# Kernel optimization log

Hardware: AMD Instinct MI355X
Metric: run time of the kernel (lower is better)

Reference implementation:

```python
import jax, jax.numpy as jnp
import numpy as np

N_NODES = 50000
N_EDGES = 800000
IN_DIM = 128
OUT_DIM = 64


def setup_inputs() -> dict:
    key = jax.random.key(0)
    k1, k2, k3, k4, k5, k6 = jax.random.split(key, 6)
    x = jax.random.normal(k1, (N_NODES, IN_DIM), dtype=jnp.float32)
    edge_row = jax.random.randint(k2, (N_EDGES,), 0, N_NODES, dtype=jnp.int32)
    edge_col = jax.random.randint(k3, (N_EDGES,), 0, N_NODES, dtype=jnp.int32)
    edge_val = jax.random.uniform(k4, (N_EDGES,), dtype=jnp.float32)
    stdv = 1.0 / np.sqrt(OUT_DIM)
    w = jax.random.uniform(k5, (IN_DIM, OUT_DIM), minval=-stdv, maxval=stdv, dtype=jnp.float32)
    b = jax.random.uniform(k6, (OUT_DIM,), minval=-stdv, maxval=stdv, dtype=jnp.float32)
    return {"x": x, "edge_row": edge_row, "edge_col": edge_col, "edge_val": edge_val, "w": w, "b": b}


def reference(x, edge_row, edge_col, edge_val, w, b):
    # dense projection: [N, in_dim] @ [in_dim, out_dim] -> [N, out_dim]
    hidden = x @ w
    # SpMM: out[r] = sum_e val[e] * hidden[col[e]] for edges with row[e] == r
    msg = hidden[edge_col] * edge_val[:, None]          # [E, out_dim]
    out = jax.ops.segment_sum(msg, edge_row, num_segments=N_NODES)
    return jax.nn.relu(out + b)
```

## Files before the change

kernel.cpp:

```cpp
#include <hip/hip_runtime.h>

#define N_NODES 50000
#define N_EDGES 800000
#define IN_DIM 128
#define OUT_DIM 64
#define CAP 64
#define PARTS 8
#define ROWS_PER_PART 6250
#define EDGES_PER_CHUNK 3125

#define GEMM_BLOCKS 784
#define BUCKET_BLOCKS (256 * PARTS)
#define TOTAL_BLOCKS (GEMM_BLOCKS + BUCKET_BLOCKS)

#define OFF_HID 0u
#define OFF_DEG 6400000u
#define OFF_BKT 6600192u

typedef short short8 __attribute__((ext_vector_type(8)));
typedef float f32x4 __attribute__((ext_vector_type(4)));
typedef float f32x2 __attribute__((ext_vector_type(2)));

__device__ __forceinline__ unsigned short bf_rne(float f) {
    unsigned u = __float_as_uint(f);
    u += 0x7fffu + ((u >> 16) & 1u);
    return (unsigned short)(u >> 16);
}
__device__ __forceinline__ float bf_lo(unsigned u) { return __uint_as_float(u << 16); }
__device__ __forceinline__ float bf_hi(unsigned u) { return __uint_as_float(u & 0xffff0000u); }

__global__ __launch_bounds__(256) void fused_kernel(
        const float* __restrict__ x, const float* __restrict__ w,
        unsigned short* __restrict__ hidb,
        const int* __restrict__ erow, const int* __restrict__ ecol,
        const float* __restrict__ eval,
        int* __restrict__ deg, int2* __restrict__ bucket) {
    if (blockIdx.x >= GEMM_BLOCKS) {
        const int bb = blockIdx.x - GEMM_BLOCKS;
        const int part = bb & (PARTS - 1);
        const int chunk = bb >> 3;
        const int rlo = part * ROWS_PER_PART;
        const int e0 = chunk * EDGES_PER_CHUNK;
        int i = threadIdx.x;
        #pragma unroll 1
        for (int trip = 0; trip < 3; ++trip, i += 1024) {
            const int eA = e0 + i,        eB = e0 + i + 256;
            const int eC = e0 + i + 512,  eD = e0 + i + 768;
            const int rA = __builtin_nontemporal_load(&erow[eA]);
            const int rB = __builtin_nontemporal_load(&erow[eB]);
            const int rC = __builtin_nontemporal_load(&erow[eC]);
            const int rD = __builtin_nontemporal_load(&erow[eD]);
            const int cA = __builtin_nontemporal_load(&ecol[eA]);
            const int cB = __builtin_nontemporal_load(&ecol[eB]);
            const int cC = __builtin_nontemporal_load(&ecol[eC]);
            const int cD = __builtin_nontemporal_load(&ecol[eD]);
            const float vA = __builtin_nontemporal_load(&eval[eA]);
            const float vB = __builtin_nontemporal_load(&eval[eB]);
            const float vC = __builtin_nontemporal_load(&eval[eC]);
            const float vD = __builtin_nontemporal_load(&eval[eD]);
            if ((unsigned)(rA - rlo) < (unsigned)ROWS_PER_PART) {
                const int pos = atomicAdd(&deg[rA], 1);
                if (pos < CAP) bucket[(size_t)rA * CAP + pos] = make_int2(cA, __float_as_int(vA));
            }
            if ((unsigned)(rB - rlo) < (unsigned)ROWS_PER_PART) {
                const int pos = atomicAdd(&deg[rB], 1);
                if (pos < CAP) bucket[(size_t)rB * CAP + pos] = make_int2(cB, __float_as_int(vB));
            }
            if ((unsigned)(rC - rlo) < (unsigned)ROWS_PER_PART) {
                const int pos = atomicAdd(&deg[rC], 1);
                if (pos < CAP) bucket[(size_t)rC * CAP + pos] = make_int2(cC, __float_as_int(vC));
            }
            if ((unsigned)(rD - rlo) < (unsigned)ROWS_PER_PART) {
                const int pos = atomicAdd(&deg[rD], 1);
                if (pos < CAP) bucket[(size_t)rD * CAP + pos] = make_int2(cD, __float_as_int(vD));
            }
        }
        if (i < EDGES_PER_CHUNK) {
            const int r = __builtin_nontemporal_load(&erow[e0 + i]);
            const int c = __builtin_nontemporal_load(&ecol[e0 + i]);
            const float v = __builtin_nontemporal_load(&eval[e0 + i]);
            if ((unsigned)(r - rlo) < (unsigned)ROWS_PER_PART) {
                const int pos = atomicAdd(&deg[r], 1);
                if (pos < CAP) bucket[(size_t)r * CAP + pos] = make_int2(c, __float_as_int(v));
            }
        }
        return;
    }

    __shared__ __attribute__((aligned(16))) unsigned short smem[16 * 64 * 8];

    const int tid = threadIdx.x;
    const int lane = tid & 63;
    const int wid = tid >> 6;

    #pragma unroll
    for (int it = 0; it < 8; ++it) {
        const int e = it * 1024 + tid * 4;
        const f32x4 wv = *(const f32x4*)(w + e);
        const int k = e >> 6;
        const int n0 = e & 63;
        const int c = k >> 5, j = k & 7, lhi = ((k >> 3) & 3) * 16;
        #pragma unroll
        for (int m = 0; m < 4; ++m) {
            const int n = n0 + m;
            const int t = n >> 4;
            const int ln = lhi + (n & 15);
            smem[((c * 4 + t) * 64 + ln) * 8 + j] = bf_rne(wv[m]);
        }
    }
    __syncthreads();

    const int group = blockIdx.x * 4 + wid;

    short8 bf[16];
    if (group < N_NODES / 16) {
        #pragma unroll
        for (int f = 0; f < 16; ++f)
            bf[f] = *(const short8*)&smem[(f * 64 + lane) * 8];
    }
    __syncthreads();

    if (group < N_NODES / 16) {
        const int node0 = group * 16;
        f32x4 acc[4] = {{0, 0, 0, 0}, {0, 0, 0, 0}, {0, 0, 0, 0}, {0, 0, 0, 0}};

        #pragma unroll
        for (int c = 0; c < 4; ++c) {
            const float* xr = x + (size_t)(node0 + (lane & 15)) * IN_DIM + c * 32 + (lane >> 4) * 8;
            const f32x4 a0 = __builtin_nontemporal_load((const f32x4*)xr);
            const f32x4 a1 = __builtin_nontemporal_load((const f32x4*)(xr + 4));
            short8 af;
            af[0] = (short)bf_rne(a0[0]); af[1] = (short)bf_rne(a0[1]);
            af[2] = (short)bf_rne(a0[2]); af[3] = (short)bf_rne(a0[3]);
            af[4] = (short)bf_rne(a1[0]); af[5] = (short)bf_rne(a1[1]);
            af[6] = (short)bf_rne(a1[2]); af[7] = (short)bf_rne(a1[3]);
            #pragma unroll
            for (int t = 0; t < 4; ++t)
                acc[t] = __builtin_amdgcn_mfma_f32_16x16x32_bf16(af, bf[c * 4 + t], acc[t], 0, 0, 0);
        }

        unsigned short* obuf = smem + wid * 1024;
        #pragma unroll
        for (int t = 0; t < 4; ++t)
            #pragma unroll
            for (int r = 0; r < 4; ++r)
                obuf[((lane >> 4) * 4 + r) * 64 + t * 16 + (lane & 15)] = bf_rne(acc[t][r]);
        const uint4 o0 = *(const uint4*)&obuf[lane * 16];
        const uint4 o1 = *(const uint4*)&obuf[lane * 16 + 8];
        char* dst = (char*)hidb + (size_t)node0 * (OUT_DIM * 2) + lane * 32;
        *(uint4*)dst = o0;
        *(uint4*)(dst + 16) = o1;
    }
}

__device__ __forceinline__ void proc8(const unsigned short* __restrict__ hidb,
                                      int2 P, int base, int eoff,
                                      int q, int l, int d, float4& acc) {
    unsigned long long u[8];
    float vv[8];
    #pragma unroll
    for (int e = 0; e < 8; ++e) {
        const int src = q * 16 + eoff + e;
        int c = __shfl(P.x, src);
        const int vi = __shfl(P.y, src);
        const bool act = (base + eoff + e) < d;
        c = act ? c : 0;
        vv[e] = act ? __int_as_float(vi) : 0.f;
        u[e] = *(const unsigned long long*)&hidb[(size_t)c * OUT_DIM + 4 * l];
    }
    #pragma unroll
    for (int e = 0; e < 8; ++e) {
        const float v = vv[e];
        const unsigned ulo = (unsigned)u[e];
        const unsigned uhi = (unsigned)(u[e] >> 32);
        acc.x = fmaf(v, bf_lo(ulo), acc.x);
        acc.y = fmaf(v, bf_hi(ulo), acc.y);
        acc.z = fmaf(v, bf_lo(uhi), acc.z);
        acc.w = fmaf(v, bf_hi(uhi), acc.w);
    }
}

__device__ __forceinline__ int2 nt_int2(const int2* p) {
    const unsigned long long v = __builtin_nontemporal_load((const unsigned long long*)p);
    return make_int2((int)(unsigned)v, (int)(unsigned)(v >> 32));
}

__global__ __launch_bounds__(256) void agg_kernel(const unsigned short* __restrict__ hidb,
                                                  const int* __restrict__ deg,
                                                  const int2* __restrict__ bucket,
                                                  const float* __restrict__ b,
                                                  float* __restrict__ out) {
    const int tid = threadIdx.x;
    const int lane = tid & 63;
    const int wid = tid >> 6;
    const int q = lane >> 4;
    const int l = lane & 15;
    const int row = blockIdx.x * 16 + wid * 4 + q;

    const int d = min(deg[row], CAP);
    const int2* __restrict__ ep = bucket + (size_t)row * CAP;

    int dmax = d;
    dmax = max(dmax, __shfl_xor(dmax, 16));
    dmax = max(dmax, __shfl_xor(dmax, 32));

    const int2 pa = nt_int2(&ep[l]);
    const int2 pb = nt_int2(&ep[16 + l]);

    float4 acc = make_float4(0.f, 0.f, 0.f, 0.f);

    proc8(hidb, pa, 0, 0, q, l, d, acc);
    if (dmax > 8)  proc8(hidb, pa, 0, 8, q, l, d, acc);
    if (dmax > 16) proc8(hidb, pb, 16, 0, q, l, d, acc);
    if (dmax > 24) proc8(hidb, pb, 16, 8, q, l, d, acc);
    for (int base = 32; base < dmax; base += 16) {
        const int2 pc = nt_int2(&ep[base + l]);
        proc8(hidb, pc, base, 0, q, l, d, acc);
        if (dmax > base + 8) proc8(hidb, pc, base, 8, q, l, d, acc);
    }

    const float2 bbv = *(const float2*)&b[4 * l];
    const float2 bbv2 = *(const float2*)&b[4 * l + 2];
    f32x2 o0, o1;
    o0[0] = fmaxf(acc.x + bbv.x, 0.f);
    o0[1] = fmaxf(acc.y + bbv.y, 0.f);
    o1[0] = fmaxf(acc.z + bbv2.x, 0.f);
    o1[1] = fmaxf(acc.w + bbv2.y, 0.f);
    float* dst = out + (size_t)row * OUT_DIM + 4 * l;
    __builtin_nontemporal_store(o0, (f32x2*)dst);
    __builtin_nontemporal_store(o1, (f32x2*)(dst + 2));
}

extern "C" void kernel_launch(void* const* d_in, const int* in_sizes, int n_in,
                              void* d_out, int out_size, void* d_ws, size_t ws_size,
                              hipStream_t stream) {
    const float* x    = (const float*)d_in[0];
    const int*   erow = (const int*)d_in[1];
    const int*   ecol = (const int*)d_in[2];
    const float* eval = (const float*)d_in[3];
    const float* w    = (const float*)d_in[4];
    const float* b    = (const float*)d_in[5];
    float* out = (float*)d_out;

    char* ws = (char*)d_ws;
    unsigned short* hidb = (unsigned short*)(ws + OFF_HID);
    int*  deg    = (int*)(ws + OFF_DEG);
    int2* bucket = (int2*)(ws + OFF_BKT);

    hipMemsetAsync(deg, 0, N_NODES * sizeof(int), stream);

    fused_kernel<<<TOTAL_BLOCKS, 256, 0, stream>>>(
        x, w, hidb, erow, ecol, eval, deg, bucket);

    agg_kernel<<<N_NODES / 16, 256, 0, stream>>>(hidb, deg, bucket, b, out);
}
```

Before: 143.8 us.

## Replace row-partitioned edge bucketing with flat one-pass edge scatter

The bucketing phase used to split rows into 8 partitions, with each block rereading its edge chunk and scattering only the edges whose row fell in its partition. That meant every edge array was read 8 times. Now each edge is read exactly once by a flat grid of 512-edge blocks that scatter directly, so the bucket and degree writes are spread across all rows instead of localised per partition. Nontemporal loads are also dropped for the edge and x reads. The cost is more random atomics and writes per block with less L2 locality, and a much larger block count.

After: 155.4 us. 1.08x slower.

```diff
diff --git a/kernel.cpp b/kernel.cpp
--- a/kernel.cpp
+++ b/kernel.cpp
@@ -5,12 +5,10 @@
 #define IN_DIM 128
 #define OUT_DIM 64
 #define CAP 64
-#define PARTS 8
-#define ROWS_PER_PART 6250
-#define EDGES_PER_CHUNK 3125
 
 #define GEMM_BLOCKS 784
-#define BUCKET_BLOCKS (256 * PARTS)
+#define EDGES_PER_BLOCK 512
+#define BUCKET_BLOCKS ((N_EDGES + EDGES_PER_BLOCK - 1) / EDGES_PER_BLOCK)
 #define TOTAL_BLOCKS (GEMM_BLOCKS + BUCKET_BLOCKS)
 
 #define OFF_HID 0u
@@ -37,52 +35,21 @@
         int* __restrict__ deg, int2* __restrict__ bucket) {
     if (blockIdx.x >= GEMM_BLOCKS) {
         const int bb = blockIdx.x - GEMM_BLOCKS;
-        const int part = bb & (PARTS - 1);
-        const int chunk = bb >> 3;
-        const int rlo = part * ROWS_PER_PART;
-        const int e0 = chunk * EDGES_PER_CHUNK;
-        int i = threadIdx.x;
-        #pragma unroll 1
-        for (int trip = 0; trip < 3; ++trip, i += 1024) {
-            const int eA = e0 + i,        eB = e0 + i + 256;
-            const int eC = e0 + i + 512,  eD = e0 + i + 768;
-            const int rA = __builtin_nontemporal_load(&erow[eA]);
-            const int rB = __builtin_nontemporal_load(&erow[eB]);
-            const int rC = __builtin_nontemporal_load(&erow[eC]);
-            const int rD = __builtin_nontemporal_load(&erow[eD]);
-            const int cA = __builtin_nontemporal_load(&ecol[eA]);
-            const int cB = __builtin_nontemporal_load(&ecol[eB]);
-            const int cC = __builtin_nontemporal_load(&ecol[eC]);
-            const int cD = __builtin_nontemporal_load(&ecol[eD]);
-            const float vA = __builtin_nontemporal_load(&eval[eA]);
-            const float vB = __builtin_nontemporal_load(&eval[eB]);
-            const float vC = __builtin_nontemporal_load(&eval[eC]);
-            const float vD = __builtin_nontemporal_load(&eval[eD]);
-            if ((unsigned)(rA - rlo) < (unsigned)ROWS_PER_PART) {
-                const int pos = atomicAdd(&deg[rA], 1);
-                if (pos < CAP) bucket[(size_t)rA * CAP + pos] = make_int2(cA, __float_as_int(vA));
-            }
-            if ((unsigned)(rB - rlo) < (unsigned)ROWS_PER_PART) {
-                const int pos = atomicAdd(&deg[rB], 1);
-                if (pos < CAP) bucket[(size_t)rB * CAP + pos] = make_int2(cB, __float_as_int(vB));
-            }
-            if ((unsigned)(rC - rlo) < (unsigned)ROWS_PER_PART) {
-                const int pos = atomicAdd(&deg[rC], 1);
-                if (pos < CAP) bucket[(size_t)rC * CAP + pos] = make_int2(cC, __float_as_int(vC));
-            }
-            if ((unsigned)(rD - rlo) < (unsigned)ROWS_PER_PART) {
-                const int pos = atomicAdd(&deg[rD], 1);
-                if (pos < CAP) bucket[(size_t)rD * CAP + pos] = make_int2(cD, __float_as_int(vD));
-            }
-        }
-        if (i < EDGES_PER_CHUNK) {
-            const int r = __builtin_nontemporal_load(&erow[e0 + i]);
-            const int c = __builtin_nontemporal_load(&ecol[e0 + i]);
-            const float v = __builtin_nontemporal_load(&eval[e0 + i]);
-            if ((unsigned)(r - rlo) < (unsigned)ROWS_PER_PART) {
-                const int pos = atomicAdd(&deg[r], 1);
-                if (pos < CAP) bucket[(size_t)r * CAP + pos] = make_int2(c, __float_as_int(v));
-            }
+        const int e0 = bb * EDGES_PER_BLOCK + threadIdx.x;
+        const int eA = e0, eB = e0 + 256;
+        const bool aok = eA < N_EDGES;
+        const bool bok = eB < N_EDGES;
+        int rA = 0, cA = 0, rB = 0, cB = 0;
+        float vA = 0.f, vB = 0.f;
+        if (aok) { rA = erow[eA]; cA = ecol[eA]; vA = eval[eA]; }
+        if (bok) { rB = erow[eB]; cB = ecol[eB]; vB = eval[eB]; }
+        if (aok) {
+            const int pos = atomicAdd(&deg[rA], 1);
+            if (pos < CAP) bucket[(size_t)rA * CAP + pos] = make_int2(cA, __float_as_int(vA));
+        }
+        if (bok) {
+            const int pos = atomicAdd(&deg[rB], 1);
+            if (pos < CAP) bucket[(size_t)rB * CAP + pos] = make_int2(cB, __float_as_int(vB));
         }
         return;
     }
@@ -127,13 +94,13 @@
         #pragma unroll
         for (int c = 0; c < 4; ++c) {
             const float* xr = x + (size_t)(node0 + (lane & 15)) * IN_DIM + c * 32 + (lane >> 4) * 8;
-            const f32x4 a0 = __builtin_nontemporal_load((const f32x4*)xr);
-            const f32x4 a1 = __builtin_nontemporal_load((const f32x4*)(xr + 4));
+            const float4 a0 = *(const float4*)xr;
+            const float4 a1 = *(const float4*)(xr + 4);
             short8 af;
-            af[0] = (short)bf_rne(a0[0]); af[1] = (short)bf_rne(a0[1]);
-            af[2] = (short)bf_rne(a0[2]); af[3] = (short)bf_rne(a0[3]);
-            af[4] = (short)bf_rne(a1[0]); af[5] = (short)bf_rne(a1[1]);
-            af[6] = (short)bf_rne(a1[2]); af[7] = (short)bf_rne(a1[3]);
+            af[0] = (short)bf_rne(a0.x); af[1] = (short)bf_rne(a0.y);
+            af[2] = (short)bf_rne(a0.z); af[3] = (short)bf_rne(a0.w);
+            af[4] = (short)bf_rne(a1.x); af[5] = (short)bf_rne(a1.y);
+            af[6] = (short)bf_rne(a1.z); af[7] = (short)bf_rne(a1.w);
             #pragma unroll
             for (int t = 0; t < 4; ++t)
                 acc[t] = __builtin_amdgcn_mfma_f32_16x16x32_bf16(af, bf[c * 4 + t], acc[t], 0, 0, 0);
```
